# Kernel tuning notes

Hardware: AMD Instinct MI355X
Metric: run time of the kernel (lower is better)

Reference implementation:

```python
import jax, jax.numpy as jnp
import numpy as np

NUM_HEADS = 12
NUM_FRAMES = 8
WINDOW = (14, 14)


def _gen_relative_position_index(ws):
    h, w = ws
    num_rel = (2 * h - 1) * (2 * w - 1) + 3
    area = h * w
    coords = np.stack(np.meshgrid(np.arange(h), np.arange(w), indexing='ij'))  # (2,h,w)
    cf = coords.reshape(2, -1)
    rel = cf[:, :, None] - cf[:, None, :]  # (2,A,A)
    rel = rel.transpose(1, 2, 0).astype(np.int64)
    rel[:, :, 0] += h - 1
    rel[:, :, 1] += w - 1
    rel[:, :, 0] *= 2 * w - 1
    idx = np.zeros((area + 1, area + 1), dtype=np.int32)
    idx[1:, 1:] = rel.sum(-1)
    idx[0, :] = num_rel - 3
    idx[:, 0] = num_rel - 2
    idx[0, 0] = num_rel - 1
    return idx


def _gen_relative_temporal_index(nf):
    c = np.arange(nf)
    return (c[:, None] - c[None, :] + nf - 1).astype(np.int32)


def setup_inputs() -> dict:
    key = jax.random.key(0)
    ks = jax.random.split(key, 8)
    B, N, C = 2, NUM_FRAMES * WINDOW[0] * WINDOW[1], 768  # N = 1568
    num_rel = (2 * WINDOW[0] - 1) * (2 * WINDOW[1] - 1) + 3  # 732
    return {
        'x': jax.random.normal(ks[0], (B, N, C), jnp.float32),
        'qkv_w': jax.random.normal(ks[1], (3 * C, C), jnp.float32) * 0.02,
        'q_bias': jax.random.normal(ks[2], (C,), jnp.float32) * 0.02,
        'v_bias': jax.random.normal(ks[3], (C,), jnp.float32) * 0.02,
        'rel_pos_table': jax.random.normal(ks[4], (num_rel, NUM_HEADS), jnp.float32) * 0.02,
        'rel_temp_table': jax.random.normal(ks[5], (2 * NUM_FRAMES - 1, NUM_HEADS), jnp.float32) * 0.02,
        'proj_w': jax.random.normal(ks[6], (C, C), jnp.float32) * 0.02,
        'proj_b': jax.random.normal(ks[7], (C,), jnp.float32) * 0.02,
        'rel_pos_index': jnp.asarray(_gen_relative_position_index(WINDOW)),
        'rel_temp_index': jnp.asarray(_gen_relative_temporal_index(NUM_FRAMES)),
    }


def reference(x, qkv_w, q_bias, v_bias, rel_pos_table, rel_temp_table, proj_w, proj_b,
              rel_pos_index, rel_temp_index):
    B, N, C = x.shape
    H = NUM_HEADS
    D = C // H
    scale = D ** -0.5
    nf = NUM_FRAMES

    # qkv projection with concat(q_bias, zeros(k), v_bias)
    qkv_bias = jnp.concatenate([q_bias, jnp.zeros_like(q_bias), v_bias])
    qkv = x @ qkv_w.T + qkv_bias  # [B,N,3C]
    qkv = qkv.reshape(B, N, 3, H, D).transpose(2, 0, 3, 1, 4)  # [3,B,H,N,D]
    q, k, v = qkv[0], qkv[1], qkv[2]

    attn = jnp.einsum('bhqd,bhkd->bhqk', q * scale, k)  # [B,H,N,N]

    # gathered 2D relative position bias, tiled over frames, sliced to N
    rel = rel_pos_table[rel_pos_index]  # [197,197,H]
    rel = jnp.transpose(rel, (2, 0, 1))[None]  # [1,H,197,197]
    rel = jnp.tile(rel, (1, 1, nf, nf))[:, :, :N, :N]
    attn = attn + rel

    # temporal bias, repeat_interleave by tokens-per-frame
    tpf = N // nf  # 196
    temp = rel_temp_table[rel_temp_index]  # [nf,nf,H]
    temp = jnp.transpose(temp, (2, 0, 1))[None]  # [1,H,nf,nf]
    temp = jnp.repeat(jnp.repeat(temp, tpf, axis=2), tpf, axis=3)  # [1,H,N,N]
    attn = attn + temp

    attn = jax.nn.softmax(attn, axis=-1)
    attn = jnp.nan_to_num(attn, nan=0.0)

    out = jnp.einsum('bhqk,bhkd->bhqd', attn, v)  # [B,H,N,D]
    out = out.transpose(0, 2, 1, 3).reshape(B, N, C)
    return out @ proj_w.T + proj_b
```

## Files before the change

kernel.cpp:

```cpp
#include <hip/hip_runtime.h>
#include <hip/hip_bf16.h>

#define NHEADS 12
#define NFRAMES 8
#define NTOK 1568
#define CDIM 768
#define DHEAD 64
#define BATCH 2
#define MROWS (BATCH * NTOK)
#define MPAD 3200
#define K3 (3 * CDIM)
#define AREA1 197
#define TPF 196
#define LOG2E 1.4426950408889634f

typedef __bf16 bf16x8 __attribute__((ext_vector_type(8)));
typedef float f32x4 __attribute__((ext_vector_type(4)));
typedef float f32x16 __attribute__((ext_vector_type(16)));
typedef unsigned short u16x8 __attribute__((ext_vector_type(8)));

#if __has_builtin(__builtin_amdgcn_exp2f)
#define EXP2(x) __builtin_amdgcn_exp2f(x)
#else
#define EXP2(x) exp2f(x)
#endif

__device__ __forceinline__ unsigned short f2bf(float f) {
  return __builtin_bit_cast(unsigned short, (__bf16)f);
}
__device__ __forceinline__ float bf2f(unsigned short u) {
  unsigned int x = ((unsigned int)u) << 16;
  return __builtin_bit_cast(float, x);
}
__device__ __forceinline__ bf16x8 ld8(const unsigned short* p) {
  return __builtin_bit_cast(bf16x8, *(const u16x8*)p);
}
__device__ __forceinline__ f32x4 mfma16(bf16x8 a, bf16x8 b, f32x4 c) {
  return __builtin_amdgcn_mfma_f32_16x16x32_bf16(a, b, c, 0, 0, 0);
}
__device__ __forceinline__ f32x16 mfma32(bf16x8 a, bf16x8 b, f32x16 c) {
  return __builtin_amdgcn_mfma_f32_32x32x16_bf16(a, b, c, 0, 0, 0);
}
__device__ __forceinline__ unsigned int pack2(float lo, float hi) {
  return ((unsigned int)f2bf(hi) << 16) | (unsigned int)f2bf(lo);
}
__device__ __forceinline__ void swap32(unsigned int a, unsigned int b,
                                       unsigned int& x, unsigned int& y) {
#if __has_builtin(__builtin_amdgcn_permlane32_swap)
  auto r = __builtin_amdgcn_permlane32_swap(a, b, false, false);
  x = r[0]; y = r[1];
#else
  const bool hi = (threadIdx.x & 63) >= 32;
  unsigned int ea = (unsigned int)__shfl_xor((int)a, 32);
  unsigned int eb = (unsigned int)__shfl_xor((int)b, 32);
  x = hi ? eb : a;
  y = hi ? b : ea;
#endif
}
#define GL_LDS(src, dst)                                                    \
  __builtin_amdgcn_global_load_lds(                                         \
      (const __attribute__((address_space(1))) void*)(src),                 \
      (__attribute__((address_space(3))) void*)(dst), 16, 0, 0)

__global__ void conv_kernel(const float* __restrict__ x,
                            const float* __restrict__ qkv_w,
                            const float* __restrict__ proj_w,
                            unsigned short* __restrict__ xb,
                            unsigned short* __restrict__ qkvwb,
                            unsigned short* __restrict__ projwb,
                            unsigned short* __restrict__ aout) {
  const int XCH = MPAD * CDIM / 4;
  const int WCH = K3 * CDIM / 4;
  const int PCH = CDIM * CDIM / 4;
  const int ACH = (MPAD - MROWS) * CDIM / 4;
  const int total = XCH + WCH + PCH + ACH;
  for (int c = blockIdx.x * blockDim.x + threadIdx.x; c < total;
       c += gridDim.x * blockDim.x) {
    if (c < XCH) {
      int m = (c * 4) / CDIM;
      float4 v = make_float4(0.f, 0.f, 0.f, 0.f);
      if (m < MROWS) v = ((const float4*)x)[c];
      ushort4 o;
      o.x = f2bf(v.x); o.y = f2bf(v.y); o.z = f2bf(v.z); o.w = f2bf(v.w);
      ((ushort4*)xb)[c] = o;
    } else if (c < XCH + WCH) {
      int c2 = c - XCH;
      float4 v = ((const float4*)qkv_w)[c2];
      ushort4 o;
      o.x = f2bf(v.x); o.y = f2bf(v.y); o.z = f2bf(v.z); o.w = f2bf(v.w);
      ((ushort4*)qkvwb)[c2] = o;
    } else if (c < XCH + WCH + PCH) {
      int c2 = c - XCH - WCH;
      float4 v = ((const float4*)proj_w)[c2];
      ushort4 o;
      o.x = f2bf(v.x); o.y = f2bf(v.y); o.z = f2bf(v.z); o.w = f2bf(v.w);
      ((ushort4*)projwb)[c2] = o;
    } else {
      int c2 = c - XCH - WCH - PCH;
      ushort4 z; z.x = 0; z.y = 0; z.z = 0; z.w = 0;
      ((ushort4*)(aout + (size_t)MROWS * CDIM))[c2] = z;
    }
  }
}

__global__ void biasP_kernel(const float* __restrict__ rpt,
                             const int* __restrict__ rpi,
                             unsigned short* __restrict__ biasP) {
  __shared__ float row[AREA1];
  const int h = blockIdx.x / AREA1;
  const int i = blockIdx.x - h * AREA1;
  for (int j = threadIdx.x; j < AREA1; j += 256)
    row[j] = rpt[rpi[i * AREA1 + j] * NHEADS + h] * LOG2E;
  __syncthreads();
  unsigned short* dst = biasP + (size_t)blockIdx.x * 49 * 32;
  for (int e = threadIdx.x; e < 49 * 32; e += 256) {
    const int t = e >> 5, r = e & 31;
    const int hi = r >> 4, rr = r & 15;
    int km = 32 * t + (rr & 3) + 8 * (rr >> 2) + 4 * hi;
    km %= AREA1;
    dst[e] = f2bf(row[km]);
  }
}

__global__ void bias2_kernel(const float* __restrict__ rtt,
                             const int* __restrict__ rti,
                             float* __restrict__ bias2) {
  int t = blockIdx.x * blockDim.x + threadIdx.x;
  if (t < NHEADS * 64) {
    int h = t >> 6, ff = t & 63;
    bias2[t] = rtt[rti[ff] * NHEADS + h] * LOG2E;
  }
}

template <int MODE, int BM, int BN>
__global__ __launch_bounds__(256) void gemm_kernel(
    const unsigned short* __restrict__ A,
    const unsigned short* __restrict__ Bw,
    const float* __restrict__ bias0,
    const float* __restrict__ biasv,
    unsigned short* __restrict__ qbuf,
    unsigned short* __restrict__ kbuf,
    unsigned short* __restrict__ vtbuf,
    float* __restrict__ Cout) {
  __shared__ unsigned short As[2][BM * 32];
  __shared__ unsigned short Bs[2][BN * 32];
  const int lane = threadIdx.x & 63;
  const int wv = threadIdx.x >> 6;
  const int tid = threadIdx.x;
  const int m0 = blockIdx.y * BM;
  const int n0 = blockIdx.x * BN;
  constexpr int WM = BM / 2, WN = BN / 2;

  auto stage = [&](int buf, int kt) {
    const int k0 = kt * 32;
#pragma unroll
    for (int ai = 0; ai < BM / 64; ++ai) {
      const int c = ai * 256 + tid;
      const int r = c >> 2, seg = c & 3;
      GL_LDS(A + (size_t)(m0 + r) * CDIM + k0 + seg * 8, &As[buf][c * 8]);
    }
#pragma unroll
    for (int bi = 0; bi < BN / 64; ++bi) {
      const int c = bi * 256 + tid;
      const int r = c >> 2, seg = c & 3;
      GL_LDS(Bw + (size_t)(n0 + r) * CDIM + k0 + seg * 8, &Bs[buf][c * 8]);
    }
  };

  f32x4 acc[WM / 16][WN / 16] = {};
  const int rbase = (wv >> 1) * WM;
  const int cbase = (wv & 1) * WN;

  stage(0, 0);
  __syncthreads();
  int cur = 0;
  for (int kt = 0; kt < CDIM / 32; ++kt) {
    if (kt + 1 < CDIM / 32) stage(cur ^ 1, kt + 1);
    bf16x8 af[WM / 16], bg[WN / 16];
#pragma unroll
    for (int i = 0; i < WM / 16; ++i)
      af[i] = ld8(&As[cur][(rbase + i * 16 + (lane & 15)) * 32 + (lane >> 4) * 8]);
#pragma unroll
    for (int j = 0; j < WN / 16; ++j)
      bg[j] = ld8(&Bs[cur][(cbase + j * 16 + (lane & 15)) * 32 + (lane >> 4) * 8]);
#pragma unroll
    for (int i = 0; i < WM / 16; ++i)
#pragma unroll
      for (int j = 0; j < WN / 16; ++j)
        acc[i][j] = mfma16(af[i], bg[j], acc[i][j]);
    __syncthreads();
    cur ^= 1;
  }

#pragma unroll
  for (int i = 0; i < WM / 16; ++i) {
#pragma unroll
    for (int j = 0; j < WN / 16; ++j) {
#pragma unroll
      for (int r = 0; r < 4; ++r) {
        int grow = m0 + rbase + i * 16 + (lane >> 4) * 4 + r;
        int gcol = n0 + cbase + j * 16 + (lane & 15);
        if (grow >= MROWS) continue;
        float v = acc[i][j][r];
        if (MODE == 0) {
          int which = gcol / CDIM;
          int cc = gcol - which * CDIM;
          int hh = cc >> 6, dd = cc & 63;
          int b = grow / NTOK, n = grow - b * NTOK;
          size_t hd = ((size_t)(b * NHEADS + hh) * NTOK + n) * 64 + dd;
          if (which == 0)
            qbuf[hd] = f2bf((v + bias0[cc]) * (0.125f * LOG2E));
          else if (which == 1)
            kbuf[hd] = f2bf(v);
          else
            vtbuf[((size_t)(b * NHEADS + hh) * 64 + dd) * NTOK + n] =
                f2bf(v + biasv[cc]);
        } else {
          Cout[(size_t)grow * CDIM + gcol] = v + bias0[gcol];
        }
      }
    }
  }
}

__global__ __launch_bounds__(256) void attn_kernel(
    const unsigned short* __restrict__ qbuf,
    const unsigned short* __restrict__ kbuf,
    const unsigned short* __restrict__ vtbuf,
    const unsigned short* __restrict__ biasP,
    const float* __restrict__ bias2,
    unsigned short* __restrict__ aout) {
  __shared__ __align__(16) char smem[36864];
  unsigned short* stg = (unsigned short*)smem;
  float* mb = (float*)smem;

  const int lane = threadIdx.x & 63;
  const int wv = threadIdx.x >> 6;
  const int wu = (blockIdx.x & 7) * 147 + (blockIdx.x >> 3);
  const int bh = wu / 49;
  const int qt = wu - bh * 49;
  const int q0 = qt * 32;
  const int h = bh % NHEADS;
  const int b = bh / NHEADS;
  const int qlane = lane & 31;
  const int hi = lane >> 5;
  const int hi4 = hi * 4;
  const int qn = q0 + qlane;
  const int qfr = qn / TPF < 7 ? qn / TPF : 7;
  const int qmod = qn % AREA1;

  const unsigned short* qp = qbuf + (size_t)bh * NTOK * DHEAD;
  const unsigned short* kp = kbuf + (size_t)bh * NTOK * DHEAD;
  const unsigned short* vp = vtbuf + (size_t)bh * DHEAD * NTOK;
  const unsigned short* bP = biasP + ((size_t)(h * AREA1 + qmod) * 49) * 32 + hi * 16;
  const float* b2q = bias2 + h * 64 + qfr * 8;

  unsigned short* KsW = stg + wv * 4096;
  unsigned short* VsW = KsW + 2048;

  const unsigned short* ksb =
      kp + (size_t)(lane >> 3) * DHEAD + (((lane & 7) ^ (lane >> 3)) << 3);
  const unsigned short* vsb =
      vp + (size_t)(lane >> 2) * NTOK + (((lane & 3) ^ ((lane >> 3) & 3)) << 3);

  auto stage = [&](int gt) {
    const int kv0 = gt * 32;
#pragma unroll
    for (int j = 0; j < 4; ++j) {
      GL_LDS(ksb + (size_t)(kv0 + j * 8) * DHEAD, KsW + j * 512);
      GL_LDS(vsb + kv0 + (size_t)(j * 16) * NTOK, VsW + j * 512);
    }
  };

  bf16x8 aq[4];
#pragma unroll
  for (int c = 0; c < 4; ++c)
    aq[c] = ld8(qp + (size_t)qn * DHEAD + c * 16 + hi * 8);

  f32x16 o0 = {}, o1 = {};
  float lrun = 0.f;

  stage(wv);
  u16x8 ubA, ubB;
  {
    const u16x8* bp = (const u16x8*)(bP + (size_t)wv * 32);
    ubA = bp[0]; ubB = bp[1];
  }
  int kfl = 0;
  float b2lo = b2q[0], b2hi = b2q[1];
  const int skey = qlane & 7;
  const int vswz = (qlane >> 1) & 3;

  for (int gt = wv; gt < 49; gt += 4) {
    asm volatile("s_waitcnt vmcnt(0)" ::: "memory");
    __builtin_amdgcn_sched_barrier(0);
    bf16x8 kf[4];
#pragma unroll
    for (int c = 0; c < 4; ++c)
      kf[c] = ld8(&KsW[qlane * 64 + ((((c << 1) + hi) ^ skey) << 3)]);
    bf16x8 vf0 = ld8(&VsW[qlane * 32 + ((hi ^ vswz) << 3)]);
    bf16x8 vf1 = ld8(&VsW[qlane * 32 + (((2 + hi) ^ vswz) << 3)]);
    bf16x8 vf2 = ld8(&VsW[(32 + qlane) * 32 + ((hi ^ vswz) << 3)]);
    bf16x8 vf3 = ld8(&VsW[(32 + qlane) * 32 + (((2 + hi) ^ vswz) << 3)]);
    asm volatile("s_waitcnt lgkmcnt(0)" ::: "memory");
    __builtin_amdgcn_sched_barrier(0);
    const bool more = (gt + 4 < 49);
    if (more) stage(gt + 4);

    f32x16 s;
#pragma unroll
    for (int r = 0; r < 16; ++r)
      s[r] = ((r < 8) ? bf2f(ubA[r]) : bf2f(ubB[r - 8])) + b2lo;
    __builtin_amdgcn_s_setprio(1);
#pragma unroll
    for (int c = 0; c < 4; ++c) s = mfma32(kf[c], aq[c], s);
    __builtin_amdgcn_s_setprio(0);

    const int ccr = (kfl + 1) * TPF - gt * 32;
    int kfln = kfl;
    float nb2lo = b2lo, nb2hi = b2hi;
    if (more) {
      const u16x8* bp = (const u16x8*)(bP + (size_t)(gt + 4) * 32);
      ubA = bp[0]; ubB = bp[1];
      kfln = ((gt + 4) * 8) / 49;
      nb2lo = b2q[kfln];
      nb2hi = b2q[kfln < 7 ? kfln + 1 : 7];
    }

    if (ccr < 32) {
      const float dlt = b2hi - b2lo;
#pragma unroll
      for (int r = 0; r < 16; ++r)
        s[r] += ((r & 3) + 8 * (r >> 2) + hi4 >= ccr) ? dlt : 0.f;
    }

#pragma unroll
    for (int r = 0; r < 16; ++r) s[r] = EXP2(s[r]);
    float ps;
    {
      float a = (s[0] + s[1]) + (s[2] + s[3]);
      float bb = (s[4] + s[5]) + (s[6] + s[7]);
      float cc = (s[8] + s[9]) + (s[10] + s[11]);
      float dd = (s[12] + s[13]) + (s[14] + s[15]);
      ps = (a + bb) + (cc + dd);
    }
    {
      unsigned int px, py;
      swap32(__builtin_bit_cast(unsigned int, ps),
             __builtin_bit_cast(unsigned int, ps), px, py);
      ps = __builtin_bit_cast(float, px) + __builtin_bit_cast(float, py);
    }
    lrun += ps;

    unsigned int dw[8];
#pragma unroll
    for (int c = 0; c < 8; ++c) dw[c] = pack2(s[2 * c], s[2 * c + 1]);
    unsigned int f0[4], f1[4];
    swap32(dw[0], dw[2], f0[0], f0[2]);
    swap32(dw[1], dw[3], f0[1], f0[3]);
    swap32(dw[4], dw[6], f1[0], f1[2]);
    swap32(dw[5], dw[7], f1[1], f1[3]);
    const bf16x8 F0 = __builtin_bit_cast(bf16x8, *(ulonglong2*)f0);
    const bf16x8 F1 = __builtin_bit_cast(bf16x8, *(ulonglong2*)f1);

    __builtin_amdgcn_s_setprio(1);
    o0 = mfma32(vf0, F0, o0);
    o0 = mfma32(vf1, F1, o0);
    o1 = mfma32(vf2, F0, o1);
    o1 = mfma32(vf3, F1, o1);
    __builtin_amdgcn_s_setprio(0);

    kfl = kfln;
    b2lo = nb2lo;
    b2hi = nb2hi;
  }

  __syncthreads();
  float* mrow = mb + (size_t)(wv * 64 + lane) * 34;
#pragma unroll
  for (int r = 0; r < 16; ++r) {
    mrow[r] = o0[r];
    mrow[16 + r] = o1[r];
  }
  mrow[32] = lrun;
  __syncthreads();
  if (wv < 2) {
    const int off = wv * 16;
    float acc[16];
#pragma unroll
    for (int r = 0; r < 16; ++r) acc[r] = 0.f;
    float L = 0.f;
#pragma unroll
    for (int w2 = 0; w2 < 4; ++w2) {
      const float* rr = mb + (size_t)(w2 * 64 + lane) * 34;
      L += rr[32];
#pragma unroll
      for (int r = 0; r < 16; ++r) acc[r] += rr[off + r];
    }
    const float rinv = 1.0f / L;
    unsigned short* op = aout + (size_t)(b * NTOK + qn) * CDIM + h * 64 + wv * 32;
#pragma unroll
    for (int c = 0; c < 8; ++c) {
      const int d0 = 8 * (c >> 1) + 4 * hi + 2 * (c & 1);
      *(unsigned int*)(op + d0) = pack2(acc[2 * c] * rinv, acc[2 * c + 1] * rinv);
    }
  }
}

extern "C" void kernel_launch(void* const* d_in, const int* in_sizes, int n_in,
                              void* d_out, int out_size, void* d_ws, size_t ws_size,
                              hipStream_t stream) {
  (void)in_sizes; (void)n_in; (void)out_size; (void)ws_size;
  const float* x        = (const float*)d_in[0];
  const float* qkv_w    = (const float*)d_in[1];
  const float* q_bias   = (const float*)d_in[2];
  const float* v_bias   = (const float*)d_in[3];
  const float* rp_table = (const float*)d_in[4];
  const float* rt_table = (const float*)d_in[5];
  const float* proj_w   = (const float*)d_in[6];
  const float* proj_b   = (const float*)d_in[7];
  const int* rp_index   = (const int*)d_in[8];
  const int* rt_index   = (const int*)d_in[9];

  char* ws = (char*)d_ws;
  unsigned short* xb     = (unsigned short*)(ws);
  unsigned short* qkvwb  = (unsigned short*)(ws + 4915200);
  unsigned short* projwb = (unsigned short*)(ws + 8454144);
  unsigned short* qbuf   = (unsigned short*)(ws + 9633792);
  unsigned short* kbuf   = (unsigned short*)(ws + 14450688);
  unsigned short* vtbuf  = (unsigned short*)(ws + 19267584);
  unsigned short* aout   = (unsigned short*)(ws + 24084480);
  unsigned short* biasP  = (unsigned short*)(ws);
  float* bias2           = (float*)(ws + 30247424);

  conv_kernel<<<2048, 256, 0, stream>>>(x, qkv_w, proj_w, xb, qkvwb, projwb, aout);
  bias2_kernel<<<3, 256, 0, stream>>>(rt_table, rt_index, bias2);
  gemm_kernel<0, 128, 64><<<dim3(K3 / 64, MPAD / 128), 256, 0, stream>>>(
      xb, qkvwb, q_bias, v_bias, qbuf, kbuf, vtbuf, nullptr);
  biasP_kernel<<<NHEADS * AREA1, 256, 0, stream>>>(rp_table, rp_index, biasP);
  attn_kernel<<<dim3(1176), 256, 0, stream>>>(
      qbuf, kbuf, vtbuf, biasP, bias2, aout);
  gemm_kernel<1, 64, 64><<<dim3(CDIM / 64, MPAD / 64), 256, 0, stream>>>(
      aout, projwb, proj_b, nullptr, nullptr, nullptr, nullptr, (float*)d_out);
}
```

Before: 124.0 us.

## Load V fragments directly from global, shrink attention LDS, fuse bias kernels

The attention kernel stops staging V through LDS. Each lane now loads its V fragments straight from global memory into registers, prefetching the next tile after the PV MFMAs. The epilogue reduction is split into two passes over a half-size LDS buffer, cutting shared memory from 36KB to 17KB to allow more resident blocks. The cross-lane row-sum swap moves out of the loop to a single final swap, and the temporal-bias kernel is folded into the biasP launch as an extra block, removing one launch. The trade-off is uncoalesced, strided V global loads and extra barriers in the epilogue.

```diff
diff --git a/kernel.cpp b/kernel.cpp
--- a/kernel.cpp
+++ b/kernel.cpp
@@ -105,7 +105,18 @@
 
 __global__ void biasP_kernel(const float* __restrict__ rpt,
                              const int* __restrict__ rpi,
-                             unsigned short* __restrict__ biasP) {
+                             const float* __restrict__ rtt,
+                             const int* __restrict__ rti,
+                             unsigned short* __restrict__ biasP,
+                             float* __restrict__ bias2) {
+  if (blockIdx.x == NHEADS * AREA1) {
+    int t = threadIdx.x;
+    for (; t < NHEADS * 64; t += 256) {
+      int h = t >> 6, ff = t & 63;
+      bias2[t] = rtt[rti[ff] * NHEADS + h] * LOG2E;
+    }
+    return;
+  }
   __shared__ float row[AREA1];
   const int h = blockIdx.x / AREA1;
   const int i = blockIdx.x - h * AREA1;
@@ -119,16 +130,6 @@
     int km = 32 * t + (rr & 3) + 8 * (rr >> 2) + 4 * hi;
     km %= AREA1;
     dst[e] = f2bf(row[km]);
-  }
-}
-
-__global__ void bias2_kernel(const float* __restrict__ rtt,
-                             const int* __restrict__ rti,
-                             float* __restrict__ bias2) {
-  int t = blockIdx.x * blockDim.x + threadIdx.x;
-  if (t < NHEADS * 64) {
-    int h = t >> 6, ff = t & 63;
-    bias2[t] = rtt[rti[ff] * NHEADS + h] * LOG2E;
   }
 }
 
@@ -230,7 +231,7 @@
     const unsigned short* __restrict__ biasP,
     const float* __restrict__ bias2,
     unsigned short* __restrict__ aout) {
-  __shared__ __align__(16) char smem[36864];
+  __shared__ __align__(16) char smem[17408];
   unsigned short* stg = (unsigned short*)smem;
   float* mb = (float*)smem;
 
@@ -255,21 +256,18 @@
   const unsigned short* bP = biasP + ((size_t)(h * AREA1 + qmod) * 49) * 32 + hi * 16;
   const float* b2q = bias2 + h * 64 + qfr * 8;
 
-  unsigned short* KsW = stg + wv * 4096;
-  unsigned short* VsW = KsW + 2048;
+  unsigned short* KsW = stg + wv * 2048;
 
   const unsigned short* ksb =
       kp + (size_t)(lane >> 3) * DHEAD + (((lane & 7) ^ (lane >> 3)) << 3);
-  const unsigned short* vsb =
-      vp + (size_t)(lane >> 2) * NTOK + (((lane & 3) ^ ((lane >> 3) & 3)) << 3);
-
-  auto stage = [&](int gt) {
+  const unsigned short* vb0 = vp + (size_t)qlane * NTOK;
+  const unsigned short* vb1 = vp + (size_t)(32 + qlane) * NTOK;
+
+  auto stageK = [&](int gt) {
     const int kv0 = gt * 32;
 #pragma unroll
-    for (int j = 0; j < 4; ++j) {
+    for (int j = 0; j < 4; ++j)
       GL_LDS(ksb + (size_t)(kv0 + j * 8) * DHEAD, KsW + j * 512);
-      GL_LDS(vsb + kv0 + (size_t)(j * 16) * NTOK, VsW + j * 512);
-    }
   };
 
   bf16x8 aq[4];
@@ -280,16 +278,23 @@
   f32x16 o0 = {}, o1 = {};
   float lrun = 0.f;
 
-  stage(wv);
+  stageK(wv);
   u16x8 ubA, ubB;
   {
     const u16x8* bp = (const u16x8*)(bP + (size_t)wv * 32);
     ubA = bp[0]; ubB = bp[1];
   }
+  bf16x8 vf0, vf1, vf2, vf3;
+  {
+    const int kv0 = wv * 32;
+    vf0 = ld8(vb0 + kv0 + hi * 8);
+    vf1 = ld8(vb0 + kv0 + 16 + hi * 8);
+    vf2 = ld8(vb1 + kv0 + hi * 8);
+    vf3 = ld8(vb1 + kv0 + 16 + hi * 8);
+  }
   int kfl = 0;
   float b2lo = b2q[0], b2hi = b2q[1];
   const int skey = qlane & 7;
-  const int vswz = (qlane >> 1) & 3;
 
   for (int gt = wv; gt < 49; gt += 4) {
     asm volatile("s_waitcnt vmcnt(0)" ::: "memory");
@@ -298,14 +303,10 @@
 #pragma unroll
     for (int c = 0; c < 4; ++c)
       kf[c] = ld8(&KsW[qlane * 64 + ((((c << 1) + hi) ^ skey) << 3)]);
-    bf16x8 vf0 = ld8(&VsW[qlane * 32 + ((hi ^ vswz) << 3)]);
-    bf16x8 vf1 = ld8(&VsW[qlane * 32 + (((2 + hi) ^ vswz) << 3)]);
-    bf16x8 vf2 = ld8(&VsW[(32 + qlane) * 32 + ((hi ^ vswz) << 3)]);
-    bf16x8 vf3 = ld8(&VsW[(32 + qlane) * 32 + (((2 + hi) ^ vswz) << 3)]);
     asm volatile("s_waitcnt lgkmcnt(0)" ::: "memory");
     __builtin_amdgcn_sched_barrier(0);
     const bool more = (gt + 4 < 49);
-    if (more) stage(gt + 4);
+    if (more) stageK(gt + 4);
 
     f32x16 s;
 #pragma unroll
@@ -336,21 +337,13 @@
 
 #pragma unroll
     for (int r = 0; r < 16; ++r) s[r] = EXP2(s[r]);
-    float ps;
     {
       float a = (s[0] + s[1]) + (s[2] + s[3]);
       float bb = (s[4] + s[5]) + (s[6] + s[7]);
       float cc = (s[8] + s[9]) + (s[10] + s[11]);
       float dd = (s[12] + s[13]) + (s[14] + s[15]);
-      ps = (a + bb) + (cc + dd);
-    }
-    {
-      unsigned int px, py;
-      swap32(__builtin_bit_cast(unsigned int, ps),
-             __builtin_bit_cast(unsigned int, ps), px, py);
-      ps = __builtin_bit_cast(float, px) + __builtin_bit_cast(float, py);
-    }
-    lrun += ps;
+      lrun += (a + bb) + (cc + dd);
+    }
 
     unsigned int dw[8];
 #pragma unroll
@@ -370,39 +363,75 @@
     o1 = mfma32(vf3, F1, o1);
     __builtin_amdgcn_s_setprio(0);
 
+    if (more) {
+      const int kv0 = (gt + 4) * 32;
+      vf0 = ld8(vb0 + kv0 + hi * 8);
+      vf1 = ld8(vb0 + kv0 + 16 + hi * 8);
+      vf2 = ld8(vb1 + kv0 + hi * 8);
+      vf3 = ld8(vb1 + kv0 + 16 + hi * 8);
+    }
+
     kfl = kfln;
     b2lo = nb2lo;
     b2hi = nb2hi;
   }
 
-  __syncthreads();
-  float* mrow = mb + (size_t)(wv * 64 + lane) * 34;
-#pragma unroll
-  for (int r = 0; r < 16; ++r) {
-    mrow[r] = o0[r];
-    mrow[16 + r] = o1[r];
-  }
-  mrow[32] = lrun;
-  __syncthreads();
+  {
+    unsigned int lx, ly;
+    swap32(__builtin_bit_cast(unsigned int, lrun),
+           __builtin_bit_cast(unsigned int, lrun), lx, ly);
+    lrun = __builtin_bit_cast(float, lx) + __builtin_bit_cast(float, ly);
+  }
+
+  __syncthreads();
+  float* mrow = mb + (size_t)(wv * 64 + lane) * 17;
+#pragma unroll
+  for (int r = 0; r < 16; ++r) mrow[r] = o0[r];
+  mrow[16] = lrun;
+  __syncthreads();
+  float L = 0.f;
   if (wv < 2) {
-    const int off = wv * 16;
+#pragma unroll
+    for (int w2 = 0; w2 < 4; ++w2) L += mb[(size_t)(w2 * 64 + lane) * 17 + 16];
+  }
+  unsigned short* op = aout + (size_t)(b * NTOK + qn) * CDIM + h * 64;
+  if (wv == 0) {
     float acc[16];
 #pragma unroll
     for (int r = 0; r < 16; ++r) acc[r] = 0.f;
-    float L = 0.f;
 #pragma unroll
     for (int w2 = 0; w2 < 4; ++w2) {
-      const float* rr = mb + (size_t)(w2 * 64 + lane) * 34;
-      L += rr[32];
-#pragma unroll
-      for (int r = 0; r < 16; ++r) acc[r] += rr[off + r];
+      const float* rr = mb + (size_t)(w2 * 64 + lane) * 17;
+#pragma unroll
+      for (int r = 0; r < 16; ++r) acc[r] += rr[r];
     }
     const float rinv = 1.0f / L;
-    unsigned short* op = aout + (size_t)(b * NTOK + qn) * CDIM + h * 64 + wv * 32;
 #pragma unroll
     for (int c = 0; c < 8; ++c) {
       const int d0 = 8 * (c >> 1) + 4 * hi + 2 * (c & 1);
       *(unsigned int*)(op + d0) = pack2(acc[2 * c] * rinv, acc[2 * c + 1] * rinv);
+    }
+  }
+  __syncthreads();
+#pragma unroll
+  for (int r = 0; r < 16; ++r) mrow[r] = o1[r];
+  __syncthreads();
+  if (wv == 1) {
+    float acc[16];
+#pragma unroll
+    for (int r = 0; r < 16; ++r) acc[r] = 0.f;
+#pragma unroll
+    for (int w2 = 0; w2 < 4; ++w2) {
+      const float* rr = mb + (size_t)(w2 * 64 + lane) * 17;
+#pragma unroll
+      for (int r = 0; r < 16; ++r) acc[r] += rr[r];
+    }
+    const float rinv = 1.0f / L;
+#pragma unroll
+    for (int c = 0; c < 8; ++c) {
+      const int d0 = 8 * (c >> 1) + 4 * hi + 2 * (c & 1);
+      *(unsigned int*)(op + 32 + d0) =
+          pack2(acc[2 * c] * rinv, acc[2 * c + 1] * rinv);
     }
   }
 }
@@ -434,10 +463,10 @@
   float* bias2           = (float*)(ws + 30247424);
 
   conv_kernel<<<2048, 256, 0, stream>>>(x, qkv_w, proj_w, xb, qkvwb, projwb, aout);
-  bias2_kernel<<<3, 256, 0, stream>>>(rt_table, rt_index, bias2);
   gemm_kernel<0, 128, 64><<<dim3(K3 / 64, MPAD / 128), 256, 0, stream>>>(
       xb, qkvwb, q_bias, v_bias, qbuf, kbuf, vtbuf, nullptr);
-  biasP_kernel<<<NHEADS * AREA1, 256, 0, stream>>>(rp_table, rp_index, biasP);
+  biasP_kernel<<<NHEADS * AREA1 + 1, 256, 0, stream>>>(
+      rp_table, rp_index, rt_table, rt_index, biasP, bias2);
   attn_kernel<<<dim3(1176), 256, 0, stream>>>(
       qbuf, kbuf, vtbuf, biasP, bias2, aout);
   gemm_kernel<1, 64, 64><<<dim3(CDIM / 64, MPAD / 64), 256, 0, stream>>>(
```

Result: no change. 126.4 us (+1.9%).
